# Kernel tuning notes

Measured on AMD Instinct MI355X. Metric: run time of the kernel, lower is better.

Reference implementation:

```python
import jax, jax.numpy as jnp
import numpy as np

D_MODEL = 1024
NHEAD = 16
D_K = D_MODEL // NHEAD


def setup_inputs() -> dict:
    key = jax.random.key(0)
    ks = jax.random.split(key, 11)
    B, S = 2, 2048
    scale = 1.0 / np.sqrt(D_MODEL)
    inp = {
        "q": jax.random.normal(ks[0], (B, S, D_MODEL), jnp.float32),
        "k": jax.random.normal(ks[1], (B, S, D_MODEL), jnp.float32),
        "v": jax.random.normal(ks[2], (B, S, D_MODEL), jnp.float32),
        "Wq": jax.random.normal(ks[3], (D_MODEL, D_MODEL), jnp.float32) * scale,
        "bq": jnp.zeros((D_MODEL,), jnp.float32),
        "Wk": jax.random.normal(ks[4], (D_MODEL, D_MODEL), jnp.float32) * scale,
        "bk": jnp.zeros((D_MODEL,), jnp.float32),
        "Wv": jax.random.normal(ks[5], (D_MODEL, D_MODEL), jnp.float32) * scale,
        "bv": jnp.zeros((D_MODEL,), jnp.float32),
        "Wo": jax.random.normal(ks[6], (D_MODEL, D_MODEL), jnp.float32) * scale,
        "bo": jnp.zeros((D_MODEL,), jnp.float32),
    }
    return inp


def reference(q, k, v, Wq, bq, Wk, bk, Wv, bv, Wo, bo):
    B, S, _ = q.shape
    # Linear projections (torch Linear: x @ W.T + b), split into heads
    def proj(x, W, b):
        y = jnp.einsum('bsd,ed->bse', x, W) + b
        return y.reshape(B, -1, NHEAD, D_K).transpose(0, 2, 1, 3)  # [B,H,S,Dk]

    qh = proj(q, Wq, bq)
    kh = proj(k, Wk, bk)
    vh = proj(v, Wv, bv)

    scores = jnp.einsum('bhqd,bhkd->bhqk', qh, kh) / jnp.sqrt(
        jnp.asarray(D_K, qh.dtype))
    attn = jax.nn.softmax(scores, axis=-1)  # dropout is identity in eval
    out = jnp.einsum('bhqk,bhkd->bhqd', attn, vh)
    out = out.transpose(0, 2, 1, 3).reshape(B, S, D_MODEL)
    return jnp.einsum('bsd,ed->bse', out, Wo) + bo
```

## Files before the change

### kernel.cpp

```cpp
#include <hip/hip_runtime.h>
#include <stdint.h>
#include <stddef.h>

#define D_MODEL 1024
#define NHEAD   16
#define DK      64
#define BB      2
#define SS      2048
#define NTOK    (BB*SS)

#define SCALE_Q 0.18033688011f

typedef short  short8 __attribute__((ext_vector_type(8)));
typedef __bf16 bf16x8 __attribute__((ext_vector_type(8)));
typedef float  f32x4  __attribute__((ext_vector_type(4)));

__device__ __forceinline__ unsigned short f2bf(float x){
  unsigned int u = __builtin_bit_cast(unsigned int, x);
  u += 0x7fffu + ((u >> 16) & 1u);
  return (unsigned short)(u >> 16);
}

__device__ __forceinline__ unsigned int pack_bf2(float x, float y){
  unsigned int a = __builtin_bit_cast(unsigned int, x) + 0x8000u;
  unsigned int b = __builtin_bit_cast(unsigned int, y) + 0x8000u;
  return __builtin_amdgcn_perm(b, a, 0x07060302u);
}

__device__ __forceinline__ float fast_exp2(float x){
#if __has_builtin(__builtin_amdgcn_exp2f)
  return __builtin_amdgcn_exp2f(x);
#else
  return exp2f(x);
#endif
}

__device__ __forceinline__ f32x4 mfma16(bf16x8 a, bf16x8 b, f32x4 c){
  return __builtin_amdgcn_mfma_f32_16x16x32_bf16(a, b, c, 0, 0, 0);
}

__device__ __forceinline__ void async16(const void* g, void* lds){
  __builtin_amdgcn_global_load_lds(
      (const __attribute__((address_space(1))) unsigned int*)g,
      (__attribute__((address_space(3))) unsigned int*)lds,
      16, 0, 0);
}

__global__ __launch_bounds__(256) void cast_bf16_all(
    const float* __restrict__ q,  const float* __restrict__ k,  const float* __restrict__ v,
    const float* __restrict__ wq, const float* __restrict__ wk, const float* __restrict__ wv,
    const float* __restrict__ wo,
    unsigned short* __restrict__ qb,  unsigned short* __restrict__ kb,  unsigned short* __restrict__ vb,
    unsigned short* __restrict__ wqb, unsigned short* __restrict__ wkb, unsigned short* __restrict__ wvb,
    unsigned short* __restrict__ wob)
{
  const float* src; unsigned short* dst; int n;
  switch (blockIdx.y){
    case 0: src = q;  dst = qb;  n = NTOK*D_MODEL;    break;
    case 1: src = k;  dst = kb;  n = NTOK*D_MODEL;    break;
    case 2: src = v;  dst = vb;  n = NTOK*D_MODEL;    break;
    case 3: src = wq; dst = wqb; n = D_MODEL*D_MODEL; break;
    case 4: src = wk; dst = wkb; n = D_MODEL*D_MODEL; break;
    case 5: src = wv; dst = wvb; n = D_MODEL*D_MODEL; break;
    default: src = wo; dst = wob; n = D_MODEL*D_MODEL; break;
  }
  int i = (blockIdx.x * 256 + threadIdx.x) * 8;
  if (i >= n) return;
  float4 a = *(const float4*)(src + i);
  float4 b = *(const float4*)(src + i + 4);
  short8 o;
  o[0] = (short)f2bf(a.x); o[1] = (short)f2bf(a.y);
  o[2] = (short)f2bf(a.z); o[3] = (short)f2bf(a.w);
  o[4] = (short)f2bf(b.x); o[5] = (short)f2bf(b.y);
  o[6] = (short)f2bf(b.z); o[7] = (short)f2bf(b.w);
  *(short8*)(dst + i) = o;
}

__global__ __launch_bounds__(256) void qkv_gemm(
    const unsigned short* __restrict__ qb, const unsigned short* __restrict__ kb,
    const unsigned short* __restrict__ vb,
    const unsigned short* __restrict__ wqb, const unsigned short* __restrict__ wkb,
    const unsigned short* __restrict__ wvb,
    const float* __restrict__ bq, const float* __restrict__ bk, const float* __restrict__ bv,
    unsigned short* __restrict__ Qh, unsigned short* __restrict__ Kh, unsigned short* __restrict__ Vt)
{
  __shared__ __align__(16) unsigned short As[128*64];
  __shared__ __align__(16) unsigned short Bs[128*64];
  const int id = blockIdx.x, z = id >> 8, r = id & 255;
  const unsigned short *A, *Bt; const float* bias; unsigned short* C;
  int bm, bn, N, brow; float scale;
  if (z == 0){ A = qb;  Bt = wqb; bias = bq; C = Qh; bm = (r>>3)*128; bn = (r&7)*128; N = 1024; brow = 0; scale = SCALE_Q; }
  else if (z == 1){ A = kb;  Bt = wkb; bias = bk; C = Kh; bm = (r>>3)*128; bn = (r&7)*128; N = 1024; brow = 0; scale = 1.0f; }
  else            { A = wvb; Bt = vb;  bias = bv; C = Vt; bm = (r&7)*128; bn = (r>>3)*128; N = 4096; brow = 1; scale = 1.0f; }
  const int K = 1024;
  const int tid  = threadIdx.x, lane = tid & 63, w = tid >> 6;
  const int quad = lane >> 4,   l16  = lane & 15;
  const int wm = w >> 1, wn = w & 1;
  const int sw = l16 & 7;
  f32x4 acc[4][4] = {};
  for (int kb_ = 0; kb_ < 16; ++kb_){
    const int k0 = kb_ << 6;
    __syncthreads();
    #pragma unroll
    for (int c = 0; c < 4; ++c){
      int chunk = (w*4 + c)*64 + lane;
      int row = chunk >> 3, c8 = chunk & 7;
      int cs = (c8 ^ (row & 7)) << 3;
      async16(A  + (size_t)(bm + row)*K + k0 + cs, (char*)As + (w*4 + c)*1024);
      async16(Bt + (size_t)(bn + row)*K + k0 + cs, (char*)Bs + (w*4 + c)*1024);
    }
    __syncthreads();
    bf16x8 af[4][2], bf[4][2];
    #pragma unroll
    for (int mt = 0; mt < 4; ++mt)
      #pragma unroll
      for (int ks = 0; ks < 2; ++ks){
        int off = (((ks*4 + quad) ^ sw) << 3);
        af[mt][ks] = *(const bf16x8*)&As[(wm*64 + mt*16 + l16)*64 + off];
        bf[mt][ks] = *(const bf16x8*)&Bs[(wn*64 + mt*16 + l16)*64 + off];
      }
    #pragma unroll
    for (int ks = 0; ks < 2; ++ks)
      #pragma unroll
      for (int mt = 0; mt < 4; ++mt)
        #pragma unroll
        for (int nt = 0; nt < 4; ++nt)
          acc[mt][nt] = mfma16(af[mt][ks], bf[nt][ks], acc[mt][nt]);
  }
  const int m0 = bm + wm*64, n0 = bn + wn*64;
  #pragma unroll
  for (int mt = 0; mt < 4; ++mt){
    #pragma unroll
    for (int nt = 0; nt < 4; ++nt){
      int col = n0 + nt*16 + l16;
      float bc = brow ? 0.0f : bias[col];
      #pragma unroll
      for (int rr = 0; rr < 4; ++rr){
        int row = m0 + mt*16 + quad*4 + rr;
        float val = (acc[mt][nt][rr] + (brow ? bias[row] : bc)) * scale;
        C[(size_t)row*N + col] = f2bf(val);
      }
    }
  }
}

__global__ __launch_bounds__(256) void gemm_out(
    const unsigned short* __restrict__ A, const unsigned short* __restrict__ Bt,
    const float* __restrict__ bias, float* __restrict__ C)
{
  __shared__ __align__(16) unsigned short As[64*64];
  __shared__ __align__(16) unsigned short Bs[128*64];
  const int K = 1024, N = 1024;
  const int tid  = threadIdx.x, lane = tid & 63, w = tid >> 6;
  const int quad = lane >> 4,   l16  = lane & 15;
  const int bm = blockIdx.y * 64, bn = blockIdx.x * 128;
  const int sw = l16 & 7;
  f32x4 acc[4][2] = {};
  for (int kb_ = 0; kb_ < 16; ++kb_){
    const int k0 = kb_ << 6;
    __syncthreads();
    #pragma unroll
    for (int c = 0; c < 2; ++c){
      int chunk = (w*2 + c)*64 + lane;
      int row = chunk >> 3, c8 = chunk & 7;
      async16(A + (size_t)(bm + row)*K + k0 + ((c8 ^ (row & 7)) << 3),
              (char*)As + (w*2 + c)*1024);
    }
    #pragma unroll
    for (int c = 0; c < 4; ++c){
      int chunk = (w*4 + c)*64 + lane;
      int row = chunk >> 3, c8 = chunk & 7;
      async16(Bt + (size_t)(bn + row)*K + k0 + ((c8 ^ (row & 7)) << 3),
              (char*)Bs + (w*4 + c)*1024);
    }
    __syncthreads();
    bf16x8 af[4][2], bf[2][2];
    #pragma unroll
    for (int mt = 0; mt < 4; ++mt)
      #pragma unroll
      for (int ks = 0; ks < 2; ++ks)
        af[mt][ks] = *(const bf16x8*)&As[(mt*16 + l16)*64 + (((ks*4 + quad) ^ sw) << 3)];
    #pragma unroll
    for (int nt = 0; nt < 2; ++nt)
      #pragma unroll
      for (int ks = 0; ks < 2; ++ks)
        bf[nt][ks] = *(const bf16x8*)&Bs[(w*32 + nt*16 + l16)*64 + (((ks*4 + quad) ^ sw) << 3)];
    #pragma unroll
    for (int ks = 0; ks < 2; ++ks)
      #pragma unroll
      for (int mt = 0; mt < 4; ++mt)
        #pragma unroll
        for (int nt = 0; nt < 2; ++nt)
          acc[mt][nt] = mfma16(af[mt][ks], bf[nt][ks], acc[mt][nt]);
  }
  #pragma unroll
  for (int mt = 0; mt < 4; ++mt){
    #pragma unroll
    for (int nt = 0; nt < 2; ++nt){
      int col = bn + w*32 + nt*16 + l16;
      float bc = bias[col];
      #pragma unroll
      for (int rr = 0; rr < 4; ++rr){
        int row = bm + mt*16 + quad*4 + rr;
        C[(size_t)row*N + col] = acc[mt][nt][rr] + bc;
      }
    }
  }
}

__global__ __launch_bounds__(256) void attn(
    const unsigned short* __restrict__ Qh, const unsigned short* __restrict__ Kh,
    const unsigned short* __restrict__ Vt, unsigned short* __restrict__ ctx)
{
  __shared__ __align__(16) unsigned short Kbuf[128*64];
  __shared__ __align__(16) unsigned short Vbuf[64*128];
  __shared__ __align__(16) unsigned short QP[128*64];

  const int tid  = threadIdx.x, lane = tid & 63, w = tid >> 6;
  const int quad = lane >> 4,   l16  = lane & 15;
  const int b = blockIdx.y >> 4, h = blockIdx.y & 15;
  const int q0 = blockIdx.x * 128;
  const int sw = l16 & 7;

  #pragma unroll
  for (int c = 0; c < 4; ++c){
    int s = (w*4 + c)*64 + lane;
    int row = s >> 3, c8 = s & 7;
    async16(Qh + (size_t)(b*SS + q0 + row)*D_MODEL + h*DK + ((c8 ^ (row & 7)) << 3),
            (char*)QP + (w*4 + c)*1024);
  }
  __syncthreads();
  bf16x8 bq0[2], bq1[2];
  #pragma unroll
  for (int ks = 0; ks < 2; ++ks){
    bq0[ks] = *(const bf16x8*)&QP[(w*32 +      l16)*64 + (((ks*4 + quad) ^ sw) << 3)];
    bq1[ks] = *(const bf16x8*)&QP[(w*32 + 16 + l16)*64 + (((ks*4 + quad) ^ sw) << 3)];
  }

  const unsigned short* Kp = Kh + (size_t)(b*SS)*D_MODEL + h*DK;
  const unsigned short* Vp = Vt + (size_t)(h*DK)*NTOK + b*SS;
  const unsigned short* ksrc[4];
  const unsigned short* vsrc[4];
  #pragma unroll
  for (int c = 0; c < 4; ++c){
    int s = (w*4 + c)*64 + lane;
    int kr = s >> 3, kc = s & 7;
    ksrc[c] = Kp + (size_t)kr*D_MODEL + ((kc ^ (kr & 7)) << 3);
    int vr = s >> 4, vc = s & 15;
    vsrc[c] = Vp + (size_t)vr*NTOK + ((vc ^ (vr & 15)) << 3);
  }

  f32x4 acc[2][4] = {};
  float l_i[2] = {0.0f, 0.0f};

  for (int it = 0; it < 16; ++it){
    __syncthreads();
    #pragma unroll
    for (int c = 0; c < 4; ++c){
      async16(ksrc[c], (char*)Kbuf + (w*4 + c)*1024);
      async16(vsrc[c], (char*)Vbuf + (w*4 + c)*1024);
      ksrc[c] += 128*D_MODEL;
      vsrc[c] += 128;
    }
    __syncthreads();

    #pragma unroll
    for (int half = 0; half < 2; ++half){
      bf16x8 kf[4][2];
      #pragma unroll
      for (int mt = 0; mt < 4; ++mt)
        #pragma unroll
        for (int ks = 0; ks < 2; ++ks)
          kf[mt][ks] = *(const bf16x8*)&Kbuf[(half*64 + mt*16 + l16)*64 + (((ks*4 + quad) ^ sw) << 3)];

      f32x4 s0[4] = {}, s1[4] = {};
      #pragma unroll
      for (int mt = 0; mt < 4; ++mt)
        #pragma unroll
        for (int ks = 0; ks < 2; ++ks){
          s0[mt] = mfma16(kf[mt][ks], bq0[ks], s0[mt]);
          s1[mt] = mfma16(kf[mt][ks], bq1[ks], s1[mt]);
        }

      float ls0 = 0.0f, ls1 = 0.0f;
      #pragma unroll
      for (int mt = 0; mt < 4; ++mt)
        #pragma unroll
        for (int rr = 0; rr < 4; ++rr){
          float p0 = fast_exp2(s0[mt][rr]); s0[mt][rr] = p0; ls0 += p0;
          float p1 = fast_exp2(s1[mt][rr]); s1[mt][rr] = p1; ls1 += p1;
        }
      l_i[0] += ls0; l_i[1] += ls1;
      const int pr0 = (w*32 +      l16)*64;
      const int pr1 = (w*32 + 16 + l16)*64;
      #pragma unroll
      for (int mt = 0; mt < 4; ++mt){
        int c8  = mt*2 + (quad >> 1);
        int off = ((c8 ^ sw) << 3) + (quad & 1)*4;
        uint2 p;
        p.x = pack_bf2(s0[mt][0], s0[mt][1]);
        p.y = pack_bf2(s0[mt][2], s0[mt][3]);
        *(uint2*)&QP[pr0 + off] = p;
        p.x = pack_bf2(s1[mt][0], s1[mt][1]);
        p.y = pack_bf2(s1[mt][2], s1[mt][3]);
        *(uint2*)&QP[pr1 + off] = p;
      }
      asm volatile("s_waitcnt lgkmcnt(0)" ::: "memory");
      bf16x8 bp0[2], bp1[2];
      #pragma unroll
      for (int ks = 0; ks < 2; ++ks){
        bp0[ks] = *(const bf16x8*)&QP[pr0 + (((ks*4 + quad) ^ sw) << 3)];
        bp1[ks] = *(const bf16x8*)&QP[pr1 + (((ks*4 + quad) ^ sw) << 3)];
      }

      #pragma unroll
      for (int nt = 0; nt < 4; ++nt){
        bf16x8 vf0, vf1;
        vf0 = *(const bf16x8*)&Vbuf[(nt*16 + l16)*128 + (((half*8 + quad)     ^ l16) << 3)];
        vf1 = *(const bf16x8*)&Vbuf[(nt*16 + l16)*128 + (((half*8 + 4 + quad) ^ l16) << 3)];
        acc[0][nt] = mfma16(vf0, bp0[0], acc[0][nt]);
        acc[1][nt] = mfma16(vf0, bp1[0], acc[1][nt]);
        acc[0][nt] = mfma16(vf1, bp0[1], acc[0][nt]);
        acc[1][nt] = mfma16(vf1, bp1[1], acc[1][nt]);
      }
    }
  }

  float inv[2];
  #pragma unroll
  for (int qg = 0; qg < 2; ++qg){
    float t = l_i[qg];
    t += __shfl_xor(t, 16);
    t += __shfl_xor(t, 32);
    inv[qg] = 1.0f / t;
  }
  #pragma unroll
  for (int qg = 0; qg < 2; ++qg){
    int pr = (w*32 + qg*16 + l16)*64;
    #pragma unroll
    for (int nt = 0; nt < 4; ++nt){
      int c8  = nt*2 + (quad >> 1);
      int off = ((c8 ^ sw) << 3) + (quad & 1)*4;
      uint2 p;
      p.x = pack_bf2(acc[qg][nt][0]*inv[qg], acc[qg][nt][1]*inv[qg]);
      p.y = pack_bf2(acc[qg][nt][2]*inv[qg], acc[qg][nt][3]*inv[qg]);
      *(uint2*)&QP[pr + off] = p;
    }
  }
  asm volatile("s_waitcnt lgkmcnt(0)" ::: "memory");
  {
    int r  = w*32 + (lane >> 1);
    int j0 = (lane & 1)*4;
    unsigned short* dst = ctx + (size_t)(b*SS + q0 + r)*D_MODEL + h*DK;
    #pragma unroll
    for (int i = 0; i < 4; ++i){
      int j = j0 + i;
      uint4 d = *(const uint4*)&QP[r*64 + ((j ^ (r & 7)) << 3)];
      *(uint4*)(dst + j*8) = d;
    }
  }
}

extern "C" void kernel_launch(void* const* d_in, const int* in_sizes, int n_in,
                              void* d_out, int out_size, void* d_ws, size_t ws_size,
                              hipStream_t stream) {
  const float* q  = (const float*)d_in[0];
  const float* k  = (const float*)d_in[1];
  const float* v  = (const float*)d_in[2];
  const float* Wq = (const float*)d_in[3];
  const float* bq = (const float*)d_in[4];
  const float* Wk = (const float*)d_in[5];
  const float* bk = (const float*)d_in[6];
  const float* Wv = (const float*)d_in[7];
  const float* bv = (const float*)d_in[8];
  const float* Wo = (const float*)d_in[9];
  const float* bo = (const float*)d_in[10];

  char* ws = (char*)d_ws;
  const size_t TOKB = (size_t)NTOK * D_MODEL * 2;
  const size_t WB   = (size_t)D_MODEL * D_MODEL * 2;
  unsigned short* qb  = (unsigned short*)ws;             ws += TOKB;
  unsigned short* kb  = (unsigned short*)ws;             ws += TOKB;
  unsigned short* vb  = (unsigned short*)ws;             ws += TOKB;
  unsigned short* wqb = (unsigned short*)ws;             ws += WB;
  unsigned short* wkb = (unsigned short*)ws;             ws += WB;
  unsigned short* wvb = (unsigned short*)ws;             ws += WB;
  unsigned short* wob = (unsigned short*)ws;             ws += WB;
  unsigned short* Qh  = (unsigned short*)ws;             ws += TOKB;
  unsigned short* Kh  = (unsigned short*)ws;             ws += TOKB;
  unsigned short* Vt  = (unsigned short*)ws;             ws += TOKB;
  unsigned short* ctx = (unsigned short*)ws;             ws += TOKB;

  cast_bf16_all<<<dim3(2048, 7), 256, 0, stream>>>(q, k, v, Wq, Wk, Wv, Wo,
                                                   qb, kb, vb, wqb, wkb, wvb, wob);
  qkv_gemm<<<dim3(768), 256, 0, stream>>>(qb, kb, vb, wqb, wkb, wvb,
                                          bq, bk, bv, Qh, Kh, Vt);
  attn<<<dim3(SS/128, BB*NHEAD), 256, 0, stream>>>(Qh, Kh, Vt, ctx);
  gemm_out<<<dim3(8, 64), 256, 0, stream>>>(ctx, wob, bo, (float*)d_out);
}
```

Measured before the change: 235.9 us.

## Double-buffer K/V tiles in attention to overlap loads with compute

```diff
diff --git a/kernel.cpp b/kernel.cpp
--- a/kernel.cpp
+++ b/kernel.cpp
@@ -212,8 +212,8 @@
     const unsigned short* __restrict__ Qh, const unsigned short* __restrict__ Kh,
     const unsigned short* __restrict__ Vt, unsigned short* __restrict__ ctx)
 {
-  __shared__ __align__(16) unsigned short Kbuf[128*64];
-  __shared__ __align__(16) unsigned short Vbuf[64*128];
+  __shared__ __align__(16) unsigned short Kbuf[2][64*64];
+  __shared__ __align__(16) unsigned short Vbuf[2][64*64];
   __shared__ __align__(16) unsigned short QP[128*64];
 
   const int tid  = threadIdx.x, lane = tid & 63, w = tid >> 6;
@@ -229,7 +229,29 @@
     async16(Qh + (size_t)(b*SS + q0 + row)*D_MODEL + h*DK + ((c8 ^ (row & 7)) << 3),
             (char*)QP + (w*4 + c)*1024);
   }
+
+  const unsigned short* Kp = Kh + (size_t)(b*SS)*D_MODEL + h*DK;
+  const unsigned short* Vp = Vt + (size_t)(h*DK)*NTOK + b*SS;
+  const unsigned short* ksrc[2];
+  const unsigned short* vsrc[2];
+  #pragma unroll
+  for (int c = 0; c < 2; ++c){
+    int s = (w*2 + c)*64 + lane;
+    int row = s >> 3, c8 = s & 7;
+    int cs = (c8 ^ (row & 7)) << 3;
+    ksrc[c] = Kp + (size_t)row*D_MODEL + cs;
+    vsrc[c] = Vp + (size_t)row*NTOK  + cs;
+  }
+
+  #pragma unroll
+  for (int c = 0; c < 2; ++c){
+    async16(ksrc[c], (char*)Kbuf[0] + (w*2 + c)*1024);
+    async16(vsrc[c], (char*)Vbuf[0] + (w*2 + c)*1024);
+    ksrc[c] += 64*D_MODEL;
+    vsrc[c] += 64;
+  }
   __syncthreads();
+
   bf16x8 bq0[2], bq1[2];
   #pragma unroll
   for (int ks = 0; ks < 2; ++ks){
@@ -237,93 +259,81 @@
     bq1[ks] = *(const bf16x8*)&QP[(w*32 + 16 + l16)*64 + (((ks*4 + quad) ^ sw) << 3)];
   }
 
-  const unsigned short* Kp = Kh + (size_t)(b*SS)*D_MODEL + h*DK;
-  const unsigned short* Vp = Vt + (size_t)(h*DK)*NTOK + b*SS;
-  const unsigned short* ksrc[4];
-  const unsigned short* vsrc[4];
-  #pragma unroll
-  for (int c = 0; c < 4; ++c){
-    int s = (w*4 + c)*64 + lane;
-    int kr = s >> 3, kc = s & 7;
-    ksrc[c] = Kp + (size_t)kr*D_MODEL + ((kc ^ (kr & 7)) << 3);
-    int vr = s >> 4, vc = s & 15;
-    vsrc[c] = Vp + (size_t)vr*NTOK + ((vc ^ (vr & 15)) << 3);
-  }
-
   f32x4 acc[2][4] = {};
   float l_i[2] = {0.0f, 0.0f};
 
-  for (int it = 0; it < 16; ++it){
-    __syncthreads();
-    #pragma unroll
-    for (int c = 0; c < 4; ++c){
-      async16(ksrc[c], (char*)Kbuf + (w*4 + c)*1024);
-      async16(vsrc[c], (char*)Vbuf + (w*4 + c)*1024);
-      ksrc[c] += 128*D_MODEL;
-      vsrc[c] += 128;
-    }
-    __syncthreads();
-
-    #pragma unroll
-    for (int half = 0; half < 2; ++half){
-      bf16x8 kf[4][2];
-      #pragma unroll
-      for (int mt = 0; mt < 4; ++mt)
-        #pragma unroll
-        for (int ks = 0; ks < 2; ++ks)
-          kf[mt][ks] = *(const bf16x8*)&Kbuf[(half*64 + mt*16 + l16)*64 + (((ks*4 + quad) ^ sw) << 3)];
-
-      f32x4 s0[4] = {}, s1[4] = {};
-      #pragma unroll
-      for (int mt = 0; mt < 4; ++mt)
-        #pragma unroll
-        for (int ks = 0; ks < 2; ++ks){
-          s0[mt] = mfma16(kf[mt][ks], bq0[ks], s0[mt]);
-          s1[mt] = mfma16(kf[mt][ks], bq1[ks], s1[mt]);
-        }
-
-      float ls0 = 0.0f, ls1 = 0.0f;
-      #pragma unroll
-      for (int mt = 0; mt < 4; ++mt)
-        #pragma unroll
-        for (int rr = 0; rr < 4; ++rr){
-          float p0 = fast_exp2(s0[mt][rr]); s0[mt][rr] = p0; ls0 += p0;
-          float p1 = fast_exp2(s1[mt][rr]); s1[mt][rr] = p1; ls1 += p1;
-        }
-      l_i[0] += ls0; l_i[1] += ls1;
-      const int pr0 = (w*32 +      l16)*64;
-      const int pr1 = (w*32 + 16 + l16)*64;
-      #pragma unroll
-      for (int mt = 0; mt < 4; ++mt){
-        int c8  = mt*2 + (quad >> 1);
-        int off = ((c8 ^ sw) << 3) + (quad & 1)*4;
-        uint2 p;
-        p.x = pack_bf2(s0[mt][0], s0[mt][1]);
-        p.y = pack_bf2(s0[mt][2], s0[mt][3]);
-        *(uint2*)&QP[pr0 + off] = p;
-        p.x = pack_bf2(s1[mt][0], s1[mt][1]);
-        p.y = pack_bf2(s1[mt][2], s1[mt][3]);
-        *(uint2*)&QP[pr1 + off] = p;
+  for (int it = 0; it < 32; ++it){
+    const int cur = it & 1;
+    #pragma unroll
+    for (int c = 0; c < 2; ++c){
+      async16(ksrc[c], (char*)Kbuf[1 - cur] + (w*2 + c)*1024);
+      async16(vsrc[c], (char*)Vbuf[1 - cur] + (w*2 + c)*1024);
+      ksrc[c] += 64*D_MODEL;
+      vsrc[c] += 64;
+    }
+    asm volatile("s_waitcnt vmcnt(4)\n\ts_barrier" ::: "memory");
+
+    const unsigned short* Kc = Kbuf[cur];
+    const unsigned short* Vc = Vbuf[cur];
+
+    bf16x8 kf[4][2];
+    #pragma unroll
+    for (int mt = 0; mt < 4; ++mt)
+      #pragma unroll
+      for (int ks = 0; ks < 2; ++ks)
+        kf[mt][ks] = *(const bf16x8*)&Kc[(mt*16 + l16)*64 + (((ks*4 + quad) ^ sw) << 3)];
+
+    f32x4 s0[4] = {}, s1[4] = {};
+    #pragma unroll
+    for (int mt = 0; mt < 4; ++mt)
+      #pragma unroll
+      for (int ks = 0; ks < 2; ++ks){
+        s0[mt] = mfma16(kf[mt][ks], bq0[ks], s0[mt]);
+        s1[mt] = mfma16(kf[mt][ks], bq1[ks], s1[mt]);
       }
-      asm volatile("s_waitcnt lgkmcnt(0)" ::: "memory");
-      bf16x8 bp0[2], bp1[2];
-      #pragma unroll
-      for (int ks = 0; ks < 2; ++ks){
-        bp0[ks] = *(const bf16x8*)&QP[pr0 + (((ks*4 + quad) ^ sw) << 3)];
-        bp1[ks] = *(const bf16x8*)&QP[pr1 + (((ks*4 + quad) ^ sw) << 3)];
+
+    float ls0 = 0.0f, ls1 = 0.0f;
+    #pragma unroll
+    for (int mt = 0; mt < 4; ++mt)
+      #pragma unroll
+      for (int rr = 0; rr < 4; ++rr){
+        float p0 = fast_exp2(s0[mt][rr]); s0[mt][rr] = p0; ls0 += p0;
+        float p1 = fast_exp2(s1[mt][rr]); s1[mt][rr] = p1; ls1 += p1;
       }
-
-      #pragma unroll
-      for (int nt = 0; nt < 4; ++nt){
-        bf16x8 vf0, vf1;
-        vf0 = *(const bf16x8*)&Vbuf[(nt*16 + l16)*128 + (((half*8 + quad)     ^ l16) << 3)];
-        vf1 = *(const bf16x8*)&Vbuf[(nt*16 + l16)*128 + (((half*8 + 4 + quad) ^ l16) << 3)];
-        acc[0][nt] = mfma16(vf0, bp0[0], acc[0][nt]);
-        acc[1][nt] = mfma16(vf0, bp1[0], acc[1][nt]);
-        acc[0][nt] = mfma16(vf1, bp0[1], acc[0][nt]);
-        acc[1][nt] = mfma16(vf1, bp1[1], acc[1][nt]);
-      }
-    }
+    l_i[0] += ls0; l_i[1] += ls1;
+    const int pr0 = (w*32 +      l16)*64;
+    const int pr1 = (w*32 + 16 + l16)*64;
+    #pragma unroll
+    for (int mt = 0; mt < 4; ++mt){
+      int c8  = mt*2 + (quad >> 1);
+      int off = ((c8 ^ sw) << 3) + (quad & 1)*4;
+      uint2 p;
+      p.x = pack_bf2(s0[mt][0], s0[mt][1]);
+      p.y = pack_bf2(s0[mt][2], s0[mt][3]);
+      *(uint2*)&QP[pr0 + off] = p;
+      p.x = pack_bf2(s1[mt][0], s1[mt][1]);
+      p.y = pack_bf2(s1[mt][2], s1[mt][3]);
+      *(uint2*)&QP[pr1 + off] = p;
+    }
+    asm volatile("s_waitcnt lgkmcnt(0)" ::: "memory");
+    bf16x8 bp0[2], bp1[2];
+    #pragma unroll
+    for (int ks = 0; ks < 2; ++ks){
+      bp0[ks] = *(const bf16x8*)&QP[pr0 + (((ks*4 + quad) ^ sw) << 3)];
+      bp1[ks] = *(const bf16x8*)&QP[pr1 + (((ks*4 + quad) ^ sw) << 3)];
+    }
+
+    #pragma unroll
+    for (int nt = 0; nt < 4; ++nt){
+      bf16x8 vf0 = *(const bf16x8*)&Vc[(nt*16 + l16)*64 + (((0*4 + quad) ^ sw) << 3)];
+      bf16x8 vf1 = *(const bf16x8*)&Vc[(nt*16 + l16)*64 + (((1*4 + quad) ^ sw) << 3)];
+      acc[0][nt] = mfma16(vf0, bp0[0], acc[0][nt]);
+      acc[1][nt] = mfma16(vf0, bp1[0], acc[1][nt]);
+      acc[0][nt] = mfma16(vf1, bp0[1], acc[0][nt]);
+      acc[1][nt] = mfma16(vf1, bp1[1], acc[1][nt]);
+    }
+
+    asm volatile("s_waitcnt lgkmcnt(0)\n\ts_barrier" ::: "memory");
   }
 
   float inv[2];
```

Measured after the change: 230.4 us. -2.3%, faster.
